# Kernel tuning notes

Hardware: AMD Instinct MI355X
Metric: run time of the kernel (lower is better)

The kernel has to match this reference:

```python
import jax, jax.numpy as jnp
import numpy as np

INPUT_DIM = 1024
UNITS = 1024

def setup_inputs() -> dict:
    key = jax.random.key(0)
    ks = jax.random.split(key, 7)
    B, S = 4, 2048
    x = jax.random.normal(ks[0], (B, S, INPUT_DIM), dtype=jnp.float32)
    # nn.Linear weights stored as [out, in]; biases [out]
    scale = 1.0 / np.sqrt(INPUT_DIM)
    Wq = jax.random.uniform(ks[1], (UNITS, INPUT_DIM), jnp.float32, -scale, scale)
    bq = jax.random.uniform(ks[2], (UNITS,), jnp.float32, -scale, scale)
    Wk = jax.random.uniform(ks[3], (UNITS, INPUT_DIM), jnp.float32, -scale, scale)
    bk = jax.random.uniform(ks[4], (UNITS,), jnp.float32, -scale, scale)
    Wv = jax.random.uniform(ks[5], (UNITS, INPUT_DIM), jnp.float32, -scale, scale)
    bv = jax.random.uniform(ks[6], (UNITS,), jnp.float32, -scale, scale)
    return {"x": x, "Wq": Wq, "bq": bq, "Wk": Wk, "bk": bk, "Wv": Wv, "bv": bv}

def reference(x, Wq, bq, Wk, bk, Wv, bv):
    # Q/K/V projections: [B,S,D] @ [D,U]
    Q = jnp.einsum('bsd,ud->bsu', x, Wq) + bq
    K = jnp.einsum('bsd,ud->bsu', x, Wk) + bk
    V = jnp.einsum('bsd,ud->bsu', x, Wv) + bv
    scores = jnp.einsum('bqu,bku->bqk', Q, K) / jnp.sqrt(jnp.float32(UNITS))
    attn = jax.nn.softmax(scores, axis=-1)
    return jnp.einsum('bqk,bku->bqu', attn, V)
```

## Files before the change

### kernel.cpp

```cpp
#include <hip/hip_runtime.h>
#include <hip/hip_cooperative_groups.h>
#include <cstdint>
#include <cstddef>

namespace cg = cooperative_groups;


typedef unsigned short ushort_t;
typedef __attribute__((ext_vector_type(8))) short short8;
typedef __attribute__((ext_vector_type(4))) float f32x4;

#define AS1 __attribute__((address_space(1)))
#define AS3 __attribute__((address_space(3)))

__device__ __forceinline__ ushort_t f2bf(float f) {
    unsigned int u = __float_as_uint(f);
    u += 0x7FFFu + ((u >> 16) & 1u);
    return (ushort_t)(u >> 16);
}

__device__ __forceinline__ void async_ld16(const void* g, unsigned lds_off) {
    __builtin_amdgcn_global_load_lds((const AS1 void*)(uintptr_t)g,
                                     (AS3 void*)(uintptr_t)lds_off,
                                     16, 0, 0);
}

__device__ __forceinline__ void panel_arrive(int* c) {
    __syncthreads();
    if (threadIdx.x == 0)
        __hip_atomic_fetch_add(c, 1, __ATOMIC_RELEASE,
                               __HIP_MEMORY_SCOPE_AGENT);
}
__device__ __forceinline__ void panel_wait(int* c, int tgt) {
    if (threadIdx.x == 0) {
        while (__hip_atomic_load(c, __ATOMIC_ACQUIRE,
                                 __HIP_MEMORY_SCOPE_AGENT) < tgt)
            __builtin_amdgcn_s_sleep(8);
    }
    __syncthreads();
}

template <int GX, int GY, int GZ, int CX, int CY>
__device__ __forceinline__ void remapC(int id, int& bx, int& by, int& bz) {
    constexpr int CZ  = (GX * GY * GZ) / (8 * CX * CY);
    constexpr int NCX = GX / CX, NCY = GY / CY;
    const int xcd = id & 7, jj = id >> 3;
    const int cx = xcd % NCX, ct = xcd / NCX;
    const int cy = ct % NCY, cz = ct / NCY;
    bx = cx * CX + (jj % CX);
    by = cy * CY + ((jj / CX) % CY);
    bz = cz * CZ + jj / (CX * CY);
}

template <typename OT, int EPI>
__device__ __forceinline__ void gemm_unit(
    ushort_t (&As)[2][8192], ushort_t (&Bs)[2][8192], float (&rs)[128],
    const ushort_t* __restrict__ A, const ushort_t* __restrict__ B,
    const float* __restrict__ b0, const float* __restrict__ b1,
    OT* __restrict__ C, int NT, int lda, int ldb, int ldc, float scale,
    int m0, int n0)
{
    constexpr int BK = 64;
    const int tid  = threadIdx.x;
    const int wave = tid >> 6;
    const int lane = tid & 63;
    const int wm = (wave >> 1) * 64;
    const int wn = (wave & 1) * 64;

    const unsigned lw  = (unsigned)(wave << 10);
    const unsigned aL0 = (unsigned)(uintptr_t)&As[0][0] + lw;
    const unsigned aL1 = (unsigned)(uintptr_t)&As[1][0] + lw;
    const unsigned bL0 = (unsigned)(uintptr_t)&Bs[0][0] + lw;
    const unsigned bL1 = (unsigned)(uintptr_t)&Bs[1][0] + lw;

    const int srow = wave * 8 + (lane >> 3);
    const int cd   = ((lane & 7) - srow) & 7;
    const ushort_t* gA = A + (size_t)(m0 + srow) * lda + cd * 8;
    const ushort_t* gB = B + (size_t)(n0 + srow) * ldb + cd * 8;

    auto stageT = [&](int t, unsigned la, unsigned lb) {
        const ushort_t* pA = gA + (size_t)t * BK;
        const ushort_t* pB = gB + (size_t)t * BK;
#pragma unroll
        for (int c = 0; c < 4; ++c) {
            async_ld16(pA + (size_t)(c * 32) * lda, la + c * 4096);
            async_ld16(pB + (size_t)(c * 32) * ldb, lb + c * 4096);
        }
    };

    const int frow = lane & 15;
    const int fg   = lane >> 4;

    f32x4 acc[4][4] = {};
    f32x4 rsm[4] = {};
    const short8 ones = { (short)0x3F80, (short)0x3F80, (short)0x3F80,
                          (short)0x3F80, (short)0x3F80, (short)0x3F80,
                          (short)0x3F80, (short)0x3F80 };

    auto computeT = [&](const ushort_t* Aw, const ushort_t* Bw) {
#pragma unroll
        for (int t2 = 0; t2 < 2; ++t2) {
            const int pa = (((t2 << 2) + fg + frow) & 7) << 3;
            short8 af[4], bf[4];
#pragma unroll
            for (int i = 0; i < 4; ++i)
                af[i] = *(const short8*)&Aw[(wm + i * 16 + frow) * BK + pa];
            if (EPI == 4 && wn == 0) {
#pragma unroll
                for (int i = 0; i < 4; ++i)
                    rsm[i] = __builtin_amdgcn_mfma_f32_16x16x32_bf16(
                        af[i], ones, rsm[i], 0, 0, 0);
            }
#pragma unroll
            for (int j = 0; j < 4; ++j)
                bf[j] = *(const short8*)&Bw[(wn + j * 16 + frow) * BK + pa];
#pragma unroll
            for (int i = 0; i < 4; ++i)
#pragma unroll
                for (int j = 0; j < 4; ++j)
                    acc[i][j] = __builtin_amdgcn_mfma_f32_16x16x32_bf16(
                        af[i], bf[j], acc[i][j], 0, 0, 0);
        }
    };

    const ushort_t* A0 = &As[0][0];
    const ushort_t* A1 = &As[1][0];
    const ushort_t* B0 = &Bs[0][0];
    const ushort_t* B1 = &Bs[1][0];

    stageT(0, aL0, bL0);
    __syncthreads();

    int t = 0;
    for (; t + 2 < NT; t += 2) {
        stageT(t + 1, aL1, bL1);
        computeT(A0, B0);
        __syncthreads();
        stageT(t + 2, aL0, bL0);
        computeT(A1, B1);
        __syncthreads();
    }
    stageT(NT - 1, aL1, bL1);
    computeT(A0, B0);
    __syncthreads();
    computeT(A1, B1);

    const int r0 = fg << 2;
    const int c0 = lane & 15;

    if (EPI == 4) {
        if (wn == 0 && c0 == 0) {
#pragma unroll
            for (int i = 0; i < 4; ++i)
#pragma unroll
                for (int r = 0; r < 4; ++r)
                    rs[wm + i * 16 + r0 + r] = rsm[i][r];
        }
        __syncthreads();
    }

#pragma unroll
    for (int i = 0; i < 4; ++i) {
        float bm[4];
        if (EPI == 2) {
#pragma unroll
            for (int r = 0; r < 4; ++r)
                bm[r] = b0[m0 + wm + i * 16 + r0 + r];
        }
        if (EPI == 4) {
#pragma unroll
            for (int r = 0; r < 4; ++r)
                bm[r] = 1.0f / rs[wm + i * 16 + r0 + r];
        }
#pragma unroll
        for (int j = 0; j < 4; ++j) {
            const int n = n0 + wn + j * 16 + c0;
            float bn = 0.f;
            if (EPI == 1) bn = (n < 1024) ? b0[n] : b1[n - 1024];
#pragma unroll
            for (int r = 0; r < 4; ++r) {
                const int m = m0 + wm + i * 16 + r0 + r;
                float v = acc[i][j][r] * scale;
                if (EPI == 1) v += bn;
                if (EPI == 2) v += bm[r];
                if (EPI == 3) v = __expf(v);
                if (EPI == 4) v *= bm[r];
                if constexpr (sizeof(OT) == 2)
                    C[(size_t)m * ldc + n] = f2bf(v);
                else
                    C[(size_t)m * ldc + n] = v;
            }
        }
    }
}

__device__ __forceinline__ void cast_unit(
    int u, const float* x, const float* Wq, const float* Wk, const float* Wv,
    ushort_t* Xb, ushort_t* Wqkb, ushort_t* Wkb, ushort_t* Wvb)
{
    const float* src; ushort_t* dst; size_t base;
    if (u < 4096)      { src = x;  dst = Xb;   base = (size_t)u * 2048; }
    else if (u < 4608) { src = Wq; dst = Wqkb; base = (size_t)(u - 4096) * 2048; }
    else if (u < 5120) { src = Wk; dst = Wkb;  base = (size_t)(u - 4608) * 2048; }
    else               { src = Wv; dst = Wvb;  base = (size_t)(u - 5120) * 2048; }
    const size_t i = base + threadIdx.x * 8;
    const f32x4 a = *(const f32x4*)(src + i);
    const f32x4 c = *(const f32x4*)(src + i + 4);
    short8 o;
    o[0] = (short)f2bf(a[0]); o[1] = (short)f2bf(a[1]);
    o[2] = (short)f2bf(a[2]); o[3] = (short)f2bf(a[3]);
    o[4] = (short)f2bf(c[0]); o[5] = (short)f2bf(c[1]);
    o[6] = (short)f2bf(c[2]); o[7] = (short)f2bf(c[3]);
    *(short8*)(dst + i) = o;
}

__global__ __launch_bounds__(256, 2) void mega(
    const float* __restrict__ x,
    const float* __restrict__ Wq, const float* __restrict__ bq,
    const float* __restrict__ Wk, const float* __restrict__ bk,
    const float* __restrict__ Wv, const float* __restrict__ bv,
    float* __restrict__ out, char* __restrict__ ws)
{
    __shared__ __align__(16) ushort_t As[2][8192];
    __shared__ __align__(16) ushort_t Bs[2][8192];
    __shared__ float rs[128];

    const size_t MB = 1ull << 20;
    ushort_t* Xb   = (ushort_t*)(ws);
    ushort_t* Wqkb = (ushort_t*)(ws + 16 * MB);
    ushort_t* Wkb  = (ushort_t*)(ws + 18 * MB);
    ushort_t* Wvb  = (ushort_t*)(ws + 20 * MB);
    int*      scnt = (int*)(ws + 22 * MB);
    ushort_t* QKb  = (ushort_t*)(ws + 32 * MB);
    ushort_t* Vt   = (ushort_t*)(ws + 64 * MB);
    ushort_t* Sc   = (ushort_t*)(ws);
    float* outp = out;

    cg::grid_group grid = cg::this_grid();
    const int gb = blockIdx.x;
    const int GS = gridDim.x;

    if (gb == 0 && threadIdx.x < 64) scnt[threadIdx.x] = 0;
    for (int u = gb; u < 5632; u += GS)
        cast_unit(u, x, Wq, Wk, Wv, Xb, Wqkb, Wkb, Wvb);
    grid.sync();

    for (int u = gb; u < 1536; u += GS) {
        int bx, by, bz;
        if (u < 1024) {
            remapC<16, 64, 1, 8, 16>(u, bx, by, bz);
            gemm_unit<ushort_t, 1>(As, Bs, rs, Xb, Wqkb, bq, bk,
                                   QKb, 16, 1024, 1024, 2048, 1.0f,
                                   by * 128, bx * 128);
        } else {
            remapC<64, 8, 1, 16, 4>(u - 1024, bx, by, bz);
            gemm_unit<ushort_t, 2>(As, Bs, rs, Wvb, Xb, bv, nullptr,
                                   Vt, 16, 1024, 1024, 8192, 1.0f,
                                   by * 128, bx * 128);
        }
        __syncthreads();
    }
    grid.sync();

    for (int u = gb; u < 1024; u += GS) {
        int bx, by, bz;
        remapC<16, 16, 4, 8, 16>(u, bx, by, bz);
        const size_t zo = (size_t)bz * 2048 * 2048;
        gemm_unit<ushort_t, 3>(As, Bs, rs, QKb + zo, QKb + 1024 + zo,
                               nullptr, nullptr,
                               Sc + zo, 16, 2048, 2048, 2048, 0.03125f,
                               by * 128, bx * 128);
        panel_arrive(&scnt[bz * 16 + by]);
    }

    for (int u = gb; u < 512; u += GS) {
        int bx, by, bz;
        remapC<8, 16, 4, 8, 8>(u, bx, by, bz);
        panel_wait(&scnt[bz * 16 + by], 16);
        gemm_unit<float, 4>(As, Bs, rs,
                            Sc + (size_t)bz * 2048 * 2048,
                            Vt + (size_t)bz * 2048,
                            nullptr, nullptr,
                            outp + (size_t)bz * 2048 * 1024,
                            32, 2048, 8192, 1024, 1.0f,
                            by * 128, bx * 128);
        __syncthreads();
    }
}

template <typename OT, int EPI, int CX, int CY>
__global__ __launch_bounds__(256, 2) void gemm_db(
    const ushort_t* __restrict__ A, const ushort_t* __restrict__ B,
    OT* __restrict__ C, int NT, int lda, int ldb, int ldc, float scale,
    long long aOffZ, long long bOffZ, long long cOffZ)
{
    __shared__ __align__(16) ushort_t As[2][8192];
    __shared__ __align__(16) ushort_t Bs[2][8192];
    __shared__ float rs[128];

    const int GX  = gridDim.x, GY = gridDim.y, GZ = gridDim.z;
    const int bid = blockIdx.x + GX * (blockIdx.y + GY * blockIdx.z);
    const int xcd = bid & 7, jj = bid >> 3;
    const int CZ  = (GX * GY * GZ) / (8 * CX * CY);
    const int NCX = GX / CX, NCY = GY / CY;
    const int cx  = xcd % NCX, ct = xcd / NCX;
    const int cy  = ct % NCY, cz = ct / NCY;
    const int bx  = cx * CX + (jj % CX);
    const int by  = cy * CY + ((jj / CX) % CY);
    const int bz  = cz * CZ + jj / (CX * CY);

    gemm_unit<OT, EPI>(As, Bs, rs,
                       A + (size_t)bz * aOffZ, B + (size_t)bz * bOffZ,
                       nullptr, nullptr,
                       C + (size_t)bz * cOffZ, NT, lda, ldb, ldc, scale,
                       by * 128, bx * 128);
}

__global__ __launch_bounds__(256, 2) void gemm_mrg(
    const ushort_t* __restrict__ Xb, const ushort_t* __restrict__ Wqkb,
    const ushort_t* __restrict__ Wvb,
    const float* __restrict__ bq, const float* __restrict__ bk,
    const float* __restrict__ bv,
    ushort_t* __restrict__ QKb, ushort_t* __restrict__ Vtp)
{
    __shared__ __align__(16) ushort_t As[2][8192];
    __shared__ __align__(16) ushort_t Bs[2][8192];
    __shared__ float rs[128];

    int bx, by, bz;
    if (blockIdx.x < 1024) {
        remapC<16, 64, 1, 8, 16>((int)blockIdx.x, bx, by, bz);
        gemm_unit<ushort_t, 1>(As, Bs, rs, Xb, Wqkb, bq, bk,
                               QKb, 16, 1024, 1024, 2048, 1.0f,
                               by * 128, bx * 128);
    } else {
        remapC<64, 8, 1, 16, 4>((int)blockIdx.x - 1024, bx, by, bz);
        gemm_unit<ushort_t, 2>(As, Bs, rs, Wvb, Xb, bv, nullptr,
                               Vtp, 16, 1024, 1024, 8192, 1.0f,
                               by * 128, bx * 128);
    }
}

__global__ __launch_bounds__(256) void cvt_all(
    const float* __restrict__ x,  const float* __restrict__ wq,
    const float* __restrict__ wk, const float* __restrict__ wv,
    ushort_t* __restrict__ xb,  ushort_t* __restrict__ wqb,
    ushort_t* __restrict__ wkb, ushort_t* __restrict__ wvb)
{
    cast_unit((int)blockIdx.x, x, wq, wk, wv, xb, wqb, wkb, wvb);
}

extern "C" void kernel_launch(void* const* d_in, const int* in_sizes, int n_in,
                              void* d_out, int out_size, void* d_ws, size_t ws_size,
                              hipStream_t stream)
{
    const float* x  = (const float*)d_in[0];
    const float* Wq = (const float*)d_in[1];
    const float* bq = (const float*)d_in[2];
    const float* Wk = (const float*)d_in[3];
    const float* bk = (const float*)d_in[4];
    const float* Wv = (const float*)d_in[5];
    const float* bv = (const float*)d_in[6];
    float* out = (float*)d_out;
    char* ws = (char*)d_ws;

    int nb = 0;
    hipError_t qe = hipOccupancyMaxActiveBlocksPerMultiprocessor(
        &nb, reinterpret_cast<const void*>(mega), 256, 0);
    if (qe == hipSuccess && nb >= 2) {
        void* args[] = { (void*)&x, (void*)&Wq, (void*)&bq, (void*)&Wk,
                         (void*)&bk, (void*)&Wv, (void*)&bv, (void*)&out,
                         (void*)&ws };
        hipError_t le = hipLaunchCooperativeKernel(
            reinterpret_cast<const void*>(mega), dim3(512), dim3(256),
            args, 0, stream);
        if (le == hipSuccess) return;
    }

    const size_t MB = 1ull << 20;
    ushort_t* Xb   = (ushort_t*)(ws);
    ushort_t* Wqkb = (ushort_t*)(ws + 16 * MB);
    ushort_t* Wvb  = (ushort_t*)(ws + 20 * MB);
    ushort_t* QKb  = (ushort_t*)(ws + 32 * MB);
    ushort_t* Vt   = (ushort_t*)(ws + 64 * MB);
    ushort_t* Sc   = (ushort_t*)(ws);

    cvt_all<<<dim3(5632), dim3(256), 0, stream>>>(
        x, Wq, Wk, Wv, Xb, Wqkb, (ushort_t*)(ws + 18 * MB), Wvb);

    gemm_mrg<<<dim3(1536), dim3(256), 0, stream>>>(
        Xb, Wqkb, Wvb, bq, bk, bv, QKb, Vt);

    gemm_db<ushort_t, 3, 8, 16><<<dim3(16, 16, 4), dim3(256), 0, stream>>>(
        QKb, QKb + 1024, Sc, 16, 2048, 2048, 2048,
        0.03125f, 2048ll * 2048, 2048ll * 2048, 2048ll * 2048);

    gemm_db<float, 4, 8, 8><<<dim3(8, 16, 4), dim3(256), 0, stream>>>(
        Sc, Vt, out, 32, 2048, 8192, 1024, 1.0f,
        2048ll * 2048, 2048ll, 2048ll * 1024);
}
```

Before: 217.5 us.

## Replace grid barrier between projection and scores with per-panel dataflow counters

Adds a MODE template to the cooperative megakernel. When the workspace is large enough, the scores buffer moves to a separate region so it no longer aliases the bf16 inputs. Projection tiles then signal per-panel counters, and score and PV tiles spin only on the panels they depend on instead of waiting at a full grid.sync. The score and PV loops are also unrolled to a fixed two units and one unit per block, assuming a grid of exactly 512. This aims to overlap the phases and remove barrier stalls, at the cost of atomic spin traffic and a larger workspace requirement.

```diff
diff --git a/kernel.cpp b/kernel.cpp
--- a/kernel.cpp
+++ b/kernel.cpp
@@ -31,12 +31,13 @@
         __hip_atomic_fetch_add(c, 1, __ATOMIC_RELEASE,
                                __HIP_MEMORY_SCOPE_AGENT);
 }
-__device__ __forceinline__ void panel_wait(int* c, int tgt) {
-    if (threadIdx.x == 0) {
-        while (__hip_atomic_load(c, __ATOMIC_ACQUIRE,
-                                 __HIP_MEMORY_SCOPE_AGENT) < tgt)
-            __builtin_amdgcn_s_sleep(8);
-    }
+__device__ __forceinline__ void spin1(int* c, int tgt) {
+    while (__hip_atomic_load(c, __ATOMIC_ACQUIRE,
+                             __HIP_MEMORY_SCOPE_AGENT) < tgt)
+        __builtin_amdgcn_s_sleep(8);
+}
+__device__ __forceinline__ void panel_wait1(int* c, int t) {
+    if (threadIdx.x == 0) spin1(c, t);
     __syncthreads();
 }
 
@@ -214,6 +215,7 @@
     *(short8*)(dst + i) = o;
 }
 
+template <int MODE>
 __global__ __launch_bounds__(256, 2) void mega(
     const float* __restrict__ x,
     const float* __restrict__ Wq, const float* __restrict__ bq,
@@ -230,17 +232,21 @@
     ushort_t* Wqkb = (ushort_t*)(ws + 16 * MB);
     ushort_t* Wkb  = (ushort_t*)(ws + 18 * MB);
     ushort_t* Wvb  = (ushort_t*)(ws + 20 * MB);
-    int*      scnt = (int*)(ws + 22 * MB);
     ushort_t* QKb  = (ushort_t*)(ws + 32 * MB);
     ushort_t* Vt   = (ushort_t*)(ws + 64 * MB);
-    ushort_t* Sc   = (ushort_t*)(ws);
+    ushort_t* Sc   = (MODE == 1) ? (ushort_t*)(ws + 80 * MB)
+                                 : (ushort_t*)(ws);
+    int* cnt = (MODE == 1) ? (int*)(ws + 120 * MB) : (int*)(ws + 22 * MB);
+    int* qkc = cnt;
+    int* vtc = cnt + 128;
+    int* scc = (MODE == 1) ? cnt + 160 : cnt;
     float* outp = out;
 
     cg::grid_group grid = cg::this_grid();
     const int gb = blockIdx.x;
     const int GS = gridDim.x;
 
-    if (gb == 0 && threadIdx.x < 64) scnt[threadIdx.x] = 0;
+    if (gb == 0 && threadIdx.x < 224) cnt[threadIdx.x] = 0;
     for (int u = gb; u < 5632; u += GS)
         cast_unit(u, x, Wq, Wk, Wv, Xb, Wqkb, Wkb, Wvb);
     grid.sync();
@@ -252,31 +258,54 @@
             gemm_unit<ushort_t, 1>(As, Bs, rs, Xb, Wqkb, bq, bk,
                                    QKb, 16, 1024, 1024, 2048, 1.0f,
                                    by * 128, bx * 128);
+            if (MODE == 1) panel_arrive(&qkc[by * 2 + (bx >= 8)]);
+            else __syncthreads();
         } else {
             remapC<64, 8, 1, 16, 4>(u - 1024, bx, by, bz);
             gemm_unit<ushort_t, 2>(As, Bs, rs, Wvb, Xb, bv, nullptr,
                                    Vt, 16, 1024, 1024, 8192, 1.0f,
                                    by * 128, bx * 128);
+            if (MODE == 1) panel_arrive(&vtc[by * 4 + (bx >> 4)]);
+            else __syncthreads();
+        }
+    }
+    if (MODE == 0) grid.sync();
+
+    {
+        int bx0, by0, bz0, bx1, by1, bz1;
+        remapC<16, 16, 4, 8, 16>(gb, bx0, by0, bz0);
+        remapC<16, 16, 4, 8, 16>(gb + 512, bx1, by1, bz1);
+        if (MODE == 1) {
+            if (threadIdx.x == 0) {
+                spin1(&qkc[(bz0 * 16 + by0) * 2], 8);
+                spin1(&qkc[(bz0 * 16 + bx0) * 2 + 1], 8);
+                spin1(&qkc[(bz1 * 16 + by1) * 2], 8);
+                spin1(&qkc[(bz1 * 16 + bx1) * 2 + 1], 8);
+            }
+            __syncthreads();
+        }
+        const size_t zo0 = (size_t)bz0 * 2048 * 2048;
+        gemm_unit<ushort_t, 3>(As, Bs, rs, QKb + zo0, QKb + 1024 + zo0,
+                               nullptr, nullptr,
+                               Sc + zo0, 16, 2048, 2048, 2048, 0.03125f,
+                               by0 * 128, bx0 * 128);
+        panel_arrive(&scc[bz0 * 16 + by0]);
+        const size_t zo1 = (size_t)bz1 * 2048 * 2048;
+        gemm_unit<ushort_t, 3>(As, Bs, rs, QKb + zo1, QKb + 1024 + zo1,
+                               nullptr, nullptr,
+                               Sc + zo1, 16, 2048, 2048, 2048, 0.03125f,
+                               by1 * 128, bx1 * 128);
+        panel_arrive(&scc[bz1 * 16 + by1]);
+    }
+
+    {
+        int bx, by, bz;
+        remapC<8, 16, 4, 8, 8>(gb, bx, by, bz);
+        if (threadIdx.x == 0) {
+            spin1(&scc[bz * 16 + by], 16);
+            if (MODE == 1) spin1(&vtc[bx * 4 + bz], 16);
         }
         __syncthreads();
-    }
-    grid.sync();
-
-    for (int u = gb; u < 1024; u += GS) {
-        int bx, by, bz;
-        remapC<16, 16, 4, 8, 16>(u, bx, by, bz);
-        const size_t zo = (size_t)bz * 2048 * 2048;
-        gemm_unit<ushort_t, 3>(As, Bs, rs, QKb + zo, QKb + 1024 + zo,
-                               nullptr, nullptr,
-                               Sc + zo, 16, 2048, 2048, 2048, 0.03125f,
-                               by * 128, bx * 128);
-        panel_arrive(&scnt[bz * 16 + by]);
-    }
-
-    for (int u = gb; u < 512; u += GS) {
-        int bx, by, bz;
-        remapC<8, 16, 4, 8, 8>(u, bx, by, bz);
-        panel_wait(&scnt[bz * 16 + by], 16);
         gemm_unit<float, 4>(As, Bs, rs,
                             Sc + (size_t)bz * 2048 * 2048,
                             Vt + (size_t)bz * 2048,
@@ -284,7 +313,6 @@
                             outp + (size_t)bz * 2048 * 1024,
                             32, 2048, 8192, 1024, 1.0f,
                             by * 128, bx * 128);
-        __syncthreads();
     }
 }
 
@@ -364,16 +392,19 @@
     float* out = (float*)d_out;
     char* ws = (char*)d_ws;
 
+    const bool big = ws_size >= (128ull << 20);
+    const void* fn = big ? reinterpret_cast<const void*>(mega<1>)
+                         : reinterpret_cast<const void*>(mega<0>);
+
     int nb = 0;
     hipError_t qe = hipOccupancyMaxActiveBlocksPerMultiprocessor(
-        &nb, reinterpret_cast<const void*>(mega), 256, 0);
+        &nb, fn, 256, 0);
     if (qe == hipSuccess && nb >= 2) {
         void* args[] = { (void*)&x, (void*)&Wq, (void*)&bq, (void*)&Wk,
                          (void*)&bk, (void*)&Wv, (void*)&bv, (void*)&out,
                          (void*)&ws };
         hipError_t le = hipLaunchCooperativeKernel(
-            reinterpret_cast<const void*>(mega), dim3(512), dim3(256),
-            args, 0, stream);
+            fn, dim3(512), dim3(256), args, 0, stream);
         if (le == hipSuccess) return;
     }
 
```

Result: faster. 213.2 us (-2.0%).

## Fold Wq·Wk into one matrix and fuse scores via X·M·Xᵀ with dataflow sync

Applied to the files above, without the earlier changes.

Rewrites the score computation algebraically: M = Wkᵀ-style product of the transposed Q and K weights is formed once, then G1 = X·M, and the scores come from G1·Xᵀ plus rank-one bias terms (x·(Wqᵀbk), x·(Wkᵀbq), bq·bk) folded into a new exp epilogue. This replaces the 2048-wide QK projection GEMM with a 1024x1024 weight product plus a 1024-wide GEMM. It also replaces the grid-wide barriers between phases with per-panel atomic counters so stages can overlap. It adds transpose and GEMV units and more counters, and it changes rounding because M is stored in bf16. The cooperative path is now gated on the workspace being at least 128 MB.

```diff
diff --git a/kernel.cpp b/kernel.cpp
--- a/kernel.cpp
+++ b/kernel.cpp
@@ -31,13 +31,10 @@
         __hip_atomic_fetch_add(c, 1, __ATOMIC_RELEASE,
                                __HIP_MEMORY_SCOPE_AGENT);
 }
-__device__ __forceinline__ void panel_wait(int* c, int tgt) {
-    if (threadIdx.x == 0) {
-        while (__hip_atomic_load(c, __ATOMIC_ACQUIRE,
-                                 __HIP_MEMORY_SCOPE_AGENT) < tgt)
-            __builtin_amdgcn_s_sleep(8);
-    }
-    __syncthreads();
+__device__ __forceinline__ void spin1(int* c, int tgt) {
+    while (__hip_atomic_load(c, __ATOMIC_ACQUIRE,
+                             __HIP_MEMORY_SCOPE_AGENT) < tgt)
+        __builtin_amdgcn_s_sleep(8);
 }
 
 template <int GX, int GY, int GZ, int CX, int CY>
@@ -162,7 +159,7 @@
 #pragma unroll
     for (int i = 0; i < 4; ++i) {
         float bm[4];
-        if (EPI == 2) {
+        if (EPI == 2 || EPI == 5) {
 #pragma unroll
             for (int r = 0; r < 4; ++r)
                 bm[r] = b0[m0 + wm + i * 16 + r0 + r];
@@ -177,14 +174,20 @@
             const int n = n0 + wn + j * 16 + c0;
             float bn = 0.f;
             if (EPI == 1) bn = (n < 1024) ? b0[n] : b1[n - 1024];
+            if (EPI == 5) bn = b1[n];
 #pragma unroll
             for (int r = 0; r < 4; ++r) {
                 const int m = m0 + wm + i * 16 + r0 + r;
-                float v = acc[i][j][r] * scale;
-                if (EPI == 1) v += bn;
-                if (EPI == 2) v += bm[r];
-                if (EPI == 3) v = __expf(v);
-                if (EPI == 4) v *= bm[r];
+                float v = acc[i][j][r];
+                if (EPI == 5) {
+                    v = __expf((v + bm[r] + bn) * scale);
+                } else {
+                    v *= scale;
+                    if (EPI == 1) v += bn;
+                    if (EPI == 2) v += bm[r];
+                    if (EPI == 3) v = __expf(v);
+                    if (EPI == 4) v *= bm[r];
+                }
                 if constexpr (sizeof(OT) == 2)
                     C[(size_t)m * ldc + n] = f2bf(v);
                 else
@@ -194,15 +197,8 @@
     }
 }
 
-__device__ __forceinline__ void cast_unit(
-    int u, const float* x, const float* Wq, const float* Wk, const float* Wv,
-    ushort_t* Xb, ushort_t* Wqkb, ushort_t* Wkb, ushort_t* Wvb)
-{
-    const float* src; ushort_t* dst; size_t base;
-    if (u < 4096)      { src = x;  dst = Xb;   base = (size_t)u * 2048; }
-    else if (u < 4608) { src = Wq; dst = Wqkb; base = (size_t)(u - 4096) * 2048; }
-    else if (u < 5120) { src = Wk; dst = Wkb;  base = (size_t)(u - 4608) * 2048; }
-    else               { src = Wv; dst = Wvb;  base = (size_t)(u - 5120) * 2048; }
+__device__ __forceinline__ void cast2048(const float* src, ushort_t* dst,
+                                         size_t base) {
     const size_t i = base + threadIdx.x * 8;
     const f32x4 a = *(const f32x4*)(src + i);
     const f32x4 c = *(const f32x4*)(src + i + 4);
@@ -212,6 +208,65 @@
     o[4] = (short)f2bf(c[0]); o[5] = (short)f2bf(c[1]);
     o[6] = (short)f2bf(c[2]); o[7] = (short)f2bf(c[3]);
     *(short8*)(dst + i) = o;
+}
+
+__device__ __forceinline__ void transpose_unit(int t, const float* W,
+                                               ushort_t* WT, ushort_t* lds) {
+    const int ti = t & 7, tj = t >> 3;
+#pragma unroll 4
+    for (int k = 0; k < 64; ++k) {
+        const int idx = threadIdx.x + k * 256;
+        const int r = idx >> 7, c = idx & 127;
+        lds[r * 128 + ((c + r) & 127)] =
+            f2bf(W[(size_t)(tj * 128 + r) * 1024 + ti * 128 + c]);
+    }
+    __syncthreads();
+#pragma unroll 4
+    for (int k = 0; k < 64; ++k) {
+        const int idx = threadIdx.x + k * 256;
+        const int rp = idx >> 7, cp = idx & 127;
+        WT[(size_t)(ti * 128 + rp) * 1024 + tj * 128 + cp] =
+            lds[cp * 128 + ((rp + cp) & 127)];
+    }
+    __syncthreads();
+}
+
+__device__ __forceinline__ void v_unit(int t, const float* Wq, const float* Wk,
+                                       const float* bq, const float* bk,
+                                       float* v1, float* v2) {
+    const int d = (t & 3) * 256 + threadIdx.x;
+    const float* W = (t < 4) ? Wq : Wk;
+    const float* b = (t < 4) ? bk : bq;
+    float acc = 0.f;
+    for (int u = 0; u < 1024; ++u)
+        acc += W[(size_t)u * 1024 + d] * b[u];
+    ((t < 4) ? v1 : v2)[d] = acc;
+}
+
+__device__ __forceinline__ void av_unit(int t, bool isAv, const float* x,
+                                        const float* v, const float* bq,
+                                        const float* bk, float* outv) {
+    const int wave = threadIdx.x >> 6, lane = threadIdx.x & 63;
+    float c = 0.f;
+    if (isAv) {
+#pragma unroll
+        for (int k = 0; k < 16; ++k)
+            c += bq[lane + 64 * k] * bk[lane + 64 * k];
+        for (int s = 1; s < 64; s <<= 1) c += __shfl_xor(c, s, 64);
+    }
+    for (int rr = 0; rr < 32; ++rr) {
+        const int row = t * 128 + wave * 32 + rr;
+        const float* xr = x + (size_t)row * 1024;
+        float a = 0.f;
+#pragma unroll
+        for (int e = 0; e < 4; ++e) {
+            const f32x4 xv = *(const f32x4*)(xr + e * 256 + lane * 4);
+            const f32x4 vv = *(const f32x4*)(v + e * 256 + lane * 4);
+            a += xv[0] * vv[0] + xv[1] * vv[1] + xv[2] * vv[2] + xv[3] * vv[3];
+        }
+        for (int s = 1; s < 64; s <<= 1) a += __shfl_xor(a, s, 64);
+        if (lane == 0) outv[row] = a + c;
+    }
 }
 
 __global__ __launch_bounds__(256, 2) void mega(
@@ -226,65 +281,106 @@
     __shared__ float rs[128];
 
     const size_t MB = 1ull << 20;
-    ushort_t* Xb   = (ushort_t*)(ws);
-    ushort_t* Wqkb = (ushort_t*)(ws + 16 * MB);
-    ushort_t* Wkb  = (ushort_t*)(ws + 18 * MB);
-    ushort_t* Wvb  = (ushort_t*)(ws + 20 * MB);
-    int*      scnt = (int*)(ws + 22 * MB);
-    ushort_t* QKb  = (ushort_t*)(ws + 32 * MB);
-    ushort_t* Vt   = (ushort_t*)(ws + 64 * MB);
-    ushort_t* Sc   = (ushort_t*)(ws);
-    float* outp = out;
+    ushort_t* Xb  = (ushort_t*)(ws);
+    ushort_t* Wvb = (ushort_t*)(ws + 20 * MB);
+    ushort_t* G1  = (ushort_t*)(ws + 32 * MB);
+    ushort_t* WqT = (ushort_t*)(ws + 48 * MB);
+    ushort_t* WkT = (ushort_t*)(ws + 50 * MB);
+    ushort_t* Mt  = (ushort_t*)(ws + 52 * MB);
+    float*    avv = (float*)(ws + 54 * MB);
+    float*    bvv = (float*)(ws + 54 * MB + 0x10000);
+    float*    v1  = (float*)(ws + 54 * MB + 0x20000);
+    float*    v2  = (float*)(ws + 54 * MB + 0x21000);
+    int*      cnt = (int*)(ws + 56 * MB);
+    int* mtc = cnt;
+    int* avc = cnt + 8;
+    int* bvc = cnt + 72;
+    int* g1c = cnt + 136;
+    int* vtc = cnt + 200;
+    int* scc = cnt + 232;
+    ushort_t* Vt = (ushort_t*)(ws + 64 * MB);
+    ushort_t* Sc = (ushort_t*)(ws + 80 * MB);
 
     cg::grid_group grid = cg::this_grid();
     const int gb = blockIdx.x;
     const int GS = gridDim.x;
 
-    if (gb == 0 && threadIdx.x < 64) scnt[threadIdx.x] = 0;
-    for (int u = gb; u < 5632; u += GS)
-        cast_unit(u, x, Wq, Wk, Wv, Xb, Wqkb, Wkb, Wvb);
+    if (gb == 0 && threadIdx.x < 296) cnt[threadIdx.x] = 0;
+    for (int u = gb; u < 4744; u += GS) {
+        if (u < 8)          v_unit(u, Wq, Wk, bq, bk, v1, v2);
+        else if (u < 4104)  cast2048(x,  Xb,  (size_t)(u - 8) * 2048);
+        else if (u < 4616)  cast2048(Wv, Wvb, (size_t)(u - 4104) * 2048);
+        else if (u < 4680)  transpose_unit(u - 4616, Wq, WqT, &Bs[0][0]);
+        else                transpose_unit(u - 4680, Wk, WkT, &Bs[0][0]);
+    }
     grid.sync();
 
-    for (int u = gb; u < 1536; u += GS) {
-        int bx, by, bz;
-        if (u < 1024) {
-            remapC<16, 64, 1, 8, 16>(u, bx, by, bz);
-            gemm_unit<ushort_t, 1>(As, Bs, rs, Xb, Wqkb, bq, bk,
-                                   QKb, 16, 1024, 1024, 2048, 1.0f,
-                                   by * 128, bx * 128);
-        } else {
-            remapC<64, 8, 1, 16, 4>(u - 1024, bx, by, bz);
+    for (int u = gb; u < 1216; u += GS) {
+        if (u < 64) {
+            const int mx = u & 7, my = u >> 3;
+            gemm_unit<ushort_t, 0>(As, Bs, rs, WkT, WqT, nullptr, nullptr,
+                                   Mt, 16, 1024, 1024, 1024, 1.0f,
+                                   my * 128, mx * 128);
+            panel_arrive(&mtc[my]);
+        } else if (u < 128) {
+            av_unit(u - 64, true, x, v1, bq, bk, avv);
+            panel_arrive(&avc[u - 64]);
+        } else if (u < 192) {
+            av_unit(u - 128, false, x, v2, bq, bk, bvv);
+            panel_arrive(&bvc[u - 128]);
+        } else if (u < 704) {
+            int bx, by, bz;
+            remapC<64, 8, 1, 16, 4>(u - 192, bx, by, bz);
             gemm_unit<ushort_t, 2>(As, Bs, rs, Wvb, Xb, bv, nullptr,
                                    Vt, 16, 1024, 1024, 8192, 1.0f,
                                    by * 128, bx * 128);
+            panel_arrive(&vtc[by * 4 + (bx >> 4)]);
+        } else {
+            int bx, by, bz;
+            remapC<8, 64, 1, 4, 16>(u - 704, bx, by, bz);
+            if (threadIdx.x == 0) spin1(&mtc[bx], 8);
+            __syncthreads();
+            gemm_unit<ushort_t, 0>(As, Bs, rs, Xb, Mt, nullptr, nullptr,
+                                   G1, 16, 1024, 1024, 1024, 1.0f,
+                                   by * 128, bx * 128);
+            panel_arrive(&g1c[by]);
+        }
+    }
+
+#pragma unroll
+    for (int q = 0; q < 2; ++q) {
+        int sx, sy, sz;
+        remapC<16, 16, 4, 8, 16>(gb + q * 512, sx, sy, sz);
+        if (threadIdx.x == 0) {
+            spin1(&g1c[sz * 16 + sy], 8);
+            spin1(&avc[sz * 16 + sy], 1);
+            spin1(&bvc[sz * 16 + sx], 1);
         }
         __syncthreads();
-    }
-    grid.sync();
-
-    for (int u = gb; u < 1024; u += GS) {
+        const size_t xo = (size_t)sz * 2048 * 1024;
+        gemm_unit<ushort_t, 5>(As, Bs, rs, G1 + xo, Xb + xo,
+                               avv + sz * 2048, bvv + sz * 2048,
+                               Sc + (size_t)sz * 2048 * 2048,
+                               16, 1024, 1024, 2048, 0.03125f,
+                               sy * 128, sx * 128);
+        panel_arrive(&scc[sz * 16 + sy]);
+    }
+
+    {
         int bx, by, bz;
-        remapC<16, 16, 4, 8, 16>(u, bx, by, bz);
-        const size_t zo = (size_t)bz * 2048 * 2048;
-        gemm_unit<ushort_t, 3>(As, Bs, rs, QKb + zo, QKb + 1024 + zo,
-                               nullptr, nullptr,
-                               Sc + zo, 16, 2048, 2048, 2048, 0.03125f,
-                               by * 128, bx * 128);
-        panel_arrive(&scnt[bz * 16 + by]);
-    }
-
-    for (int u = gb; u < 512; u += GS) {
-        int bx, by, bz;
-        remapC<8, 16, 4, 8, 8>(u, bx, by, bz);
-        panel_wait(&scnt[bz * 16 + by], 16);
+        remapC<8, 16, 4, 8, 8>(gb, bx, by, bz);
+        if (threadIdx.x == 0) {
+            spin1(&scc[bz * 16 + by], 16);
+            spin1(&vtc[bx * 4 + bz], 16);
+        }
+        __syncthreads();
         gemm_unit<float, 4>(As, Bs, rs,
                             Sc + (size_t)bz * 2048 * 2048,
                             Vt + (size_t)bz * 2048,
                             nullptr, nullptr,
-                            outp + (size_t)bz * 2048 * 1024,
+                            out + (size_t)bz * 2048 * 1024,
                             32, 2048, 8192, 1024, 1.0f,
                             by * 128, bx * 128);
-        __syncthreads();
     }
 }
 
@@ -347,7 +443,11 @@
     ushort_t* __restrict__ xb,  ushort_t* __restrict__ wqb,
     ushort_t* __restrict__ wkb, ushort_t* __restrict__ wvb)
 {
-    cast_unit((int)blockIdx.x, x, wq, wk, wv, xb, wqb, wkb, wvb);
+    const int b = blockIdx.x;
+    if (b < 4096)      cast2048(x,  xb,  (size_t)b * 2048);
+    else if (b < 4608) cast2048(wq, wqb, (size_t)(b - 4096) * 2048);
+    else if (b < 5120) cast2048(wk, wkb, (size_t)(b - 4608) * 2048);
+    else               cast2048(wv, wvb, (size_t)(b - 5120) * 2048);
 }
 
 extern "C" void kernel_launch(void* const* d_in, const int* in_sizes, int n_in,
@@ -364,17 +464,19 @@
     float* out = (float*)d_out;
     char* ws = (char*)d_ws;
 
-    int nb = 0;
-    hipError_t qe = hipOccupancyMaxActiveBlocksPerMultiprocessor(
-        &nb, reinterpret_cast<const void*>(mega), 256, 0);
-    if (qe == hipSuccess && nb >= 2) {
-        void* args[] = { (void*)&x, (void*)&Wq, (void*)&bq, (void*)&Wk,
-                         (void*)&bk, (void*)&Wv, (void*)&bv, (void*)&out,
-                         (void*)&ws };
-        hipError_t le = hipLaunchCooperativeKernel(
-            reinterpret_cast<const void*>(mega), dim3(512), dim3(256),
-            args, 0, stream);
-        if (le == hipSuccess) return;
+    if (ws_size >= (128ull << 20)) {
+        int nb = 0;
+        hipError_t qe = hipOccupancyMaxActiveBlocksPerMultiprocessor(
+            &nb, reinterpret_cast<const void*>(mega), 256, 0);
+        if (qe == hipSuccess && nb >= 2) {
+            void* args[] = { (void*)&x, (void*)&Wq, (void*)&bq, (void*)&Wk,
+                             (void*)&bk, (void*)&Wv, (void*)&bv, (void*)&out,
+                             (void*)&ws };
+            hipError_t le = hipLaunchCooperativeKernel(
+                reinterpret_cast<const void*>(mega), dim3(512), dim3(256),
+                args, 0, stream);
+            if (le == hipSuccess) return;
+        }
     }
 
     const size_t MB = 1ull << 20;
```

Result: no change. 219.7 us (+1.0%).
